# Kernel tuning notes

Measured on AMD Instinct MI355X. Metric: run time of the kernel, lower is better.

Reference implementation:

```python
import jax, jax.numpy as jnp
import numpy as np

D_MODEL = 256
N_HEAD = 8
D_FF = 1024
B = 8
N_PER = 4096
NQ = B * N_PER
L = 16
NEG_INF = -1e9
EPS = 1e-5


def layer_norm(x, g, b):
    mu = jnp.mean(x, axis=-1, keepdims=True)
    var = jnp.mean(jnp.square(x - mu), axis=-1, keepdims=True)
    return (x - mu) * jax.lax.rsqrt(var + EPS) * g + b


def setup_inputs() -> dict:
    key = jax.random.key(0)
    ks = jax.random.split(key, 20)
    s = 1.0 / np.sqrt(D_MODEL)
    sf = 1.0 / np.sqrt(D_FF)
    inp = {
        "src": jax.random.normal(ks[0], (NQ, D_MODEL), jnp.float32),
        "pos": jax.random.normal(ks[1], (NQ, D_MODEL), jnp.float32),
        # per-batch-relative neighbor indices in [-1, N_PER); -1 == invalid/padded
        "index_pair": jax.random.randint(ks[2], (NQ, L), 0, N_PER + 1, jnp.int32) - 1,
        "query_batch_cnt": jnp.full((B,), N_PER, jnp.int32),
        "key_batch_cnt": jnp.full((B,), N_PER, jnp.int32),
        "index_pair_batch": (jnp.arange(NQ, dtype=jnp.int32) // N_PER).astype(jnp.int32),
        "Wq": jax.random.normal(ks[3], (D_MODEL, D_MODEL), jnp.float32) * s,
        "bq": jnp.zeros((D_MODEL,), jnp.float32),
        "Wk": jax.random.normal(ks[4], (D_MODEL, D_MODEL), jnp.float32) * s,
        "bk": jnp.zeros((D_MODEL,), jnp.float32),
        "Wv": jax.random.normal(ks[5], (D_MODEL, D_MODEL), jnp.float32) * s,
        "bv": jnp.zeros((D_MODEL,), jnp.float32),
        "Wo": jax.random.normal(ks[6], (D_MODEL, D_MODEL), jnp.float32) * s,
        "bo": jnp.zeros((D_MODEL,), jnp.float32),
        "W1": jax.random.normal(ks[7], (D_MODEL, D_FF), jnp.float32) * s,
        "b1": jnp.zeros((D_FF,), jnp.float32),
        "W2": jax.random.normal(ks[8], (D_FF, D_MODEL), jnp.float32) * sf,
        "b2": jnp.zeros((D_MODEL,), jnp.float32),
        "g1": jnp.ones((D_MODEL,), jnp.float32),
        "be1": jnp.zeros((D_MODEL,), jnp.float32),
        "g2": jnp.ones((D_MODEL,), jnp.float32),
        "be2": jnp.zeros((D_MODEL,), jnp.float32),
    }
    return inp


def local_attn(q, k, v, index_pair, key_batch_cnt, index_pair_batch,
               Wq, bq, Wk, bk, Wv, bv, Wo, bo):
    H, hd = N_HEAD, D_MODEL // N_HEAD
    scale = 1.0 / np.sqrt(hd)
    qh = (q @ Wq + bq).reshape(NQ, H, hd) * scale        # [Nq,H,hd]
    kh = (k @ Wk + bk).reshape(NQ, H, hd)                # [Nk,H,hd] (Nk==Nq)
    vh = (v @ Wv + bv).reshape(NQ, H, hd)
    # start offset of each batch's keys in the stacked key tensor
    offs = jnp.cumsum(key_batch_cnt) - key_batch_cnt      # [B]
    valid = index_pair >= 0                               # [Nq,L]
    gidx = jnp.where(valid, index_pair + offs[index_pair_batch][:, None], 0)
    k_g = kh[gidx]                                        # [Nq,L,H,hd]
    v_g = vh[gidx]                                        # [Nq,L,H,hd]
    logits = jnp.einsum('nhd,nlhd->nhl', qh, k_g)         # [Nq,H,L]
    logits = jnp.where(valid[:, None, :], logits, NEG_INF)
    attn = jax.nn.softmax(logits, axis=-1)
    out = jnp.einsum('nhl,nlhd->nhd', attn, v_g).reshape(NQ, D_MODEL)
    return out @ Wo + bo


def reference(src, pos, index_pair, query_batch_cnt, key_batch_cnt, index_pair_batch,
              Wq, bq, Wk, bk, Wv, bv, Wo, bo, W1, b1, W2, b2, g1, be1, g2, be2):
    # forward_post (normalize_before=False), dropout==0 (eval)
    qk = src + pos
    src2 = local_attn(qk, qk, src, index_pair, key_batch_cnt, index_pair_batch,
                      Wq, bq, Wk, bk, Wv, bv, Wo, bo)
    x = layer_norm(src + src2, g1, be1)
    ff = jax.nn.relu(x @ W1 + b1) @ W2 + b2
    return layer_norm(x + ff, g2, be2)
```

## Files before the change

kernel.cpp:

```cpp
#include <hip/hip_runtime.h>
#include <hip/hip_bf16.h>
#include <cstdint>
#include <cstddef>

#define NQ_ 32768
#define DM_ 256
#define DFF_ 1024
#define LNB_ 16
#define NB_ 8

typedef __attribute__((ext_vector_type(4))) float f32x4;
typedef __attribute__((ext_vector_type(8))) short s16x8;

__device__ __forceinline__ float bf2f(ushort u) {
    union { unsigned int i; float f; } c; c.i = ((unsigned int)u) << 16; return c.f;
}
__device__ __forceinline__ ushort f2bf(float f) {
    union { float f; unsigned int i; } c; c.f = f;
    unsigned int x = c.i;
    return (ushort)((x + 0x7fffu + ((x >> 16) & 1u)) >> 16);
}


__global__ __launch_bounds__(256) void prep_qk(const float* __restrict__ src, const float* __restrict__ pos,
                                               ushort* __restrict__ qkb, ushort* __restrict__ srcb) {
    int i = (blockIdx.x * 256 + threadIdx.x) * 4;
    float4 s = *(const float4*)(src + i);
    float4 p = *(const float4*)(pos + i);
    ushort4 a, b;
    a.x = f2bf(s.x + p.x); a.y = f2bf(s.y + p.y); a.z = f2bf(s.z + p.z); a.w = f2bf(s.w + p.w);
    b.x = f2bf(s.x);       b.y = f2bf(s.y);       b.z = f2bf(s.z);       b.w = f2bf(s.w);
    *(ushort4*)(qkb + i) = a;
    *(ushort4*)(srcb + i) = b;
}

__global__ __launch_bounds__(256) void prep_weights(const float* __restrict__ Wq, const float* __restrict__ Wk,
                                                    const float* __restrict__ Wv, const float* __restrict__ Wo,
                                                    const float* __restrict__ W1, const float* __restrict__ W2,
                                                    const int* __restrict__ kbc,
                                                    const float* __restrict__ bq, const float* __restrict__ bk,
                                                    ushort* __restrict__ WqT, ushort* __restrict__ WkT,
                                                    ushort* __restrict__ WvT, ushort* __restrict__ WoT,
                                                    ushort* __restrict__ W1T, ushort* __restrict__ W2T,
                                                    int* __restrict__ offs, float* __restrict__ bias2) {
    const int b = blockIdx.x;
    const int t = threadIdx.x;
    if (b == 3072) {
        if (t == 0) { int a = 0; for (int i = 0; i < NB_; ++i) { offs[i] = a; a += kbc[i]; } }
        bias2[t] = bq[t];
        bias2[256 + t] = bk[t];
        return;
    }
    const float* W; ushort* Wt; int base, ks, ns;
    if (b < 1024) {
        const int sec = b >> 8;
        W  = sec == 0 ? Wq  : sec == 1 ? Wk  : sec == 2 ? Wv  : Wo;
        Wt = sec == 0 ? WqT : sec == 1 ? WkT : sec == 2 ? WvT : WoT;
        base = (b & 255) * 256; ks = 8; ns = 8;
    } else if (b < 2048) {
        W = W1; Wt = W1T; base = (b - 1024) * 256; ks = 8; ns = 10;
    } else {
        W = W2; Wt = W2T; base = (b - 2048) * 256; ks = 10; ns = 8;
    }
    const int i = base + t;
    const int n = i >> ks, k = i & ((1 << ks) - 1);
    Wt[i] = f2bf(W[(k << ns) + n]);
}


__device__ __forceinline__ void gld_lds16(const ushort* g, ushort* l) {
    __builtin_amdgcn_global_load_lds((const __attribute__((address_space(1))) void*)g,
                                     (__attribute__((address_space(3))) void*)l, 16, 0, 0);
}

template <bool RELU>
__global__ __launch_bounds__(256) void gemm_kernel(const ushort* __restrict__ A, const ushort* __restrict__ Bt,
                                                   const float* __restrict__ bias, ushort* __restrict__ C,
                                                   int M, int N, int K, float alpha) {
    __shared__ __align__(16) ushort As[2 * 128 * 32];
    __shared__ __align__(16) ushort Bs[2 * 128 * 32];
    const int tid = threadIdx.x;
    const int lane = tid & 63;
    const int wave = tid >> 6;
    const int wr = wave >> 1, wc = wave & 1;

    const int b = (int)(blockIdx.y * gridDim.x + blockIdx.x);
    const int idx = b >> 3;
    const int xt = (b & 7) * 32 + (idx & 31);
    const int yt = idx >> 5;
    const long m0 = (long)xt * 128;
    const long n0 = (long)yt * 128;

    f32x4 acc[4][4] = {};

    const int c0 = tid, c1 = tid + 256;
    const int ar0 = c0 >> 2, ac0 = c0 & 3;
    const int ar1 = c1 >> 2, ac1 = c1 & 3;
    const int as0 = (ac0 ^ ((ar0 >> 1) & 3)) * 8;
    const int as1 = (ac1 ^ ((ar1 >> 1) & 3)) * 8;
    const int la = lane & 15;
    const int sx = ((lane >> 4) ^ ((la >> 1) & 3)) * 8;

    const ushort* Ar0 = A + (m0 + ar0) * K + as0;
    const ushort* Ar1 = A + (m0 + ar1) * K + as1;
    const ushort* Br0 = Bt + (n0 + ar0) * K + as0;
    const ushort* Br1 = Bt + (n0 + ar1) * K + as1;

    const int nt = K >> 5;
    int boff = 0;
    gld_lds16(Ar0, As + c0 * 8);
    gld_lds16(Ar1, As + c1 * 8);
    gld_lds16(Br0, Bs + c0 * 8);
    gld_lds16(Br1, Bs + c1 * 8);

    for (int t = 0; t < nt; ++t) {
        if (t + 1 < nt) {
            const int kt = (t + 1) << 5;
            const int nb = boff ^ 4096;
            gld_lds16(Ar0 + kt, As + nb + c0 * 8);
            gld_lds16(Ar1 + kt, As + nb + c1 * 8);
            gld_lds16(Br0 + kt, Bs + nb + c0 * 8);
            gld_lds16(Br1 + kt, Bs + nb + c1 * 8);
            asm volatile("s_waitcnt vmcnt(4)" ::: "memory");
        } else {
            asm volatile("s_waitcnt vmcnt(0)" ::: "memory");
        }
        __builtin_amdgcn_s_barrier();
        s16x8 af[4], bfr[4];
#pragma unroll
        for (int m = 0; m < 4; ++m)
            af[m] = *(const s16x8*)(As + boff + (wr * 64 + m * 16 + la) * 32 + sx);
#pragma unroll
        for (int n = 0; n < 4; ++n)
            bfr[n] = *(const s16x8*)(Bs + boff + (wc * 64 + n * 16 + la) * 32 + sx);
        asm volatile("s_waitcnt lgkmcnt(0)" ::: "memory");
        __builtin_amdgcn_s_barrier();
#pragma unroll
        for (int m = 0; m < 4; ++m)
#pragma unroll
            for (int n = 0; n < 4; ++n)
                acc[m][n] = __builtin_amdgcn_mfma_f32_16x16x32_bf16(af[m], bfr[n], acc[m][n], 0, 0, 0);
        boff ^= 4096;
    }

#pragma unroll
    for (int n = 0; n < 4; ++n) {
        const long col = n0 + wc * 64 + n * 16 + la;
        const float bv = bias[col];
#pragma unroll
        for (int m = 0; m < 4; ++m) {
#pragma unroll
            for (int j = 0; j < 4; ++j) {
                const long row = m0 + wr * 64 + m * 16 + (lane >> 4) * 4 + j;
                float r = (acc[m][n][j] + bv) * alpha;
                if (RELU) r = fmaxf(r, 0.f);
                C[row * N + col] = f2bf(r);
            }
        }
    }
}


__global__ __launch_bounds__(256, 4) void attn_kernel(const ushort* __restrict__ QKb,
                                                      const ushort* __restrict__ Vb, const int* __restrict__ ipair,
                                                      const int* __restrict__ ipb, const int* __restrict__ offs,
                                                      ushort* __restrict__ Ob) {
    const int blk = (blockIdx.x & 7) * (NQ_ / 8 / 8) + (blockIdx.x >> 3);
    const int lane = threadIdx.x & 63;
    const int n = blk * 8 + (threadIdx.x >> 6) * 2 + (lane >> 5);
    const size_t hoff = (size_t)(lane & 31) * 8;

    float q[8];
    {
        s16x8 v = *(const s16x8*)(QKb + (size_t)n * 512 + hoff);
#pragma unroll
        for (int e = 0; e < 8; ++e) q[e] = bf2f((ushort)v[e]);
    }
    const int off = offs[ipb[n]];
    int gi[LNB_];
    float lg[LNB_];
#pragma unroll
    for (int j = 0; j < LNB_; ++j) {
        const int ip = ipair[n * LNB_ + j];
        const int g = ip >= 0 ? ip + off : 0;
        gi[j] = g;
        s16x8 v = *(const s16x8*)(QKb + (size_t)g * 512 + 256 + hoff);
        float p = 0.f;
#pragma unroll
        for (int e = 0; e < 8; ++e)
            p = fmaf(q[e], bf2f((ushort)v[e]), p);
        p += __shfl_xor(p, 1);
        p += __shfl_xor(p, 2);
        lg[j] = ip >= 0 ? p * 0.17677669529663688f : -1e9f;
    }
    float mx = lg[0];
#pragma unroll
    for (int j = 1; j < LNB_; ++j) mx = fmaxf(mx, lg[j]);
    float sum = 0.f, pw[LNB_];
#pragma unroll
    for (int j = 0; j < LNB_; ++j) { pw[j] = __expf(lg[j] - mx); sum += pw[j]; }
    const float inv = 1.f / sum;

    float acc[8] = {};
#pragma unroll
    for (int j = 0; j < LNB_; ++j) {
        s16x8 v = *(const s16x8*)(Vb + (size_t)gi[j] * DM_ + hoff);
        const float w = pw[j] * inv;
#pragma unroll
        for (int e = 0; e < 8; ++e)
            acc[e] = fmaf(w, bf2f((ushort)v[e]), acc[e]);
    }
    s16x8 o;
#pragma unroll
    for (int e = 0; e < 8; ++e) o[e] = (short)f2bf(acc[e]);
    *(s16x8*)(Ob + (size_t)n * DM_ + hoff) = o;
}


__global__ __launch_bounds__(256) void ln1_kernel(const ushort* __restrict__ a, const ushort* __restrict__ y,
                                                  const float* __restrict__ g, const float* __restrict__ be,
                                                  ushort* __restrict__ out) {
    const int row = blockIdx.x * 4 + (threadIdx.x >> 6);
    const int lane = threadIdx.x & 63;
    const int e = lane * 4;
    const size_t base = (size_t)row * DM_ + e;
    ushort4 av = *(const ushort4*)(a + base);
    ushort4 yv = *(const ushort4*)(y + base);
    float v0 = bf2f(av.x) + bf2f(yv.x), v1 = bf2f(av.y) + bf2f(yv.y);
    float v2 = bf2f(av.z) + bf2f(yv.z), v3 = bf2f(av.w) + bf2f(yv.w);
    float s = v0 + v1 + v2 + v3;
#pragma unroll
    for (int mk = 1; mk < 64; mk <<= 1) s += __shfl_xor(s, mk);
    const float mu = s * (1.f / 256.f);
    v0 -= mu; v1 -= mu; v2 -= mu; v3 -= mu;
    float qv = v0 * v0 + v1 * v1 + v2 * v2 + v3 * v3;
#pragma unroll
    for (int mk = 1; mk < 64; mk <<= 1) qv += __shfl_xor(qv, mk);
    const float r = rsqrtf(qv * (1.f / 256.f) + 1e-5f);
    ushort4 o;
    o.x = f2bf(v0 * r * g[e] + be[e]);
    o.y = f2bf(v1 * r * g[e + 1] + be[e + 1]);
    o.z = f2bf(v2 * r * g[e + 2] + be[e + 2]);
    o.w = f2bf(v3 * r * g[e + 3] + be[e + 3]);
    *(ushort4*)(out + base) = o;
}

__global__ __launch_bounds__(256) void ln2_kernel(const ushort* __restrict__ x, const ushort* __restrict__ f,
                                                  const float* __restrict__ g, const float* __restrict__ be,
                                                  float* __restrict__ out) {
    const int row = blockIdx.x * 4 + (threadIdx.x >> 6);
    const int lane = threadIdx.x & 63;
    const int e = lane * 4;
    const size_t base = (size_t)row * DM_ + e;
    ushort4 xv = *(const ushort4*)(x + base);
    ushort4 fv = *(const ushort4*)(f + base);
    float v0 = bf2f(xv.x) + bf2f(fv.x), v1 = bf2f(xv.y) + bf2f(fv.y);
    float v2 = bf2f(xv.z) + bf2f(fv.z), v3 = bf2f(xv.w) + bf2f(fv.w);
    float s = v0 + v1 + v2 + v3;
#pragma unroll
    for (int mk = 1; mk < 64; mk <<= 1) s += __shfl_xor(s, mk);
    const float mu = s * (1.f / 256.f);
    v0 -= mu; v1 -= mu; v2 -= mu; v3 -= mu;
    float qv = v0 * v0 + v1 * v1 + v2 * v2 + v3 * v3;
#pragma unroll
    for (int mk = 1; mk < 64; mk <<= 1) qv += __shfl_xor(qv, mk);
    const float r = rsqrtf(qv * (1.f / 256.f) + 1e-5f);
    float4 o;
    o.x = v0 * r * g[e] + be[e];
    o.y = v1 * r * g[e + 1] + be[e + 1];
    o.z = v2 * r * g[e + 2] + be[e + 2];
    o.w = v3 * r * g[e + 3] + be[e + 3];
    *(float4*)(out + base) = o;
}


extern "C" void kernel_launch(void* const* d_in, const int* in_sizes, int n_in,
                              void* d_out, int out_size, void* d_ws, size_t ws_size,
                              hipStream_t stream) {
    const float* src = (const float*)d_in[0];
    const float* pos = (const float*)d_in[1];
    const int* ipair = (const int*)d_in[2];
    const int* kbc   = (const int*)d_in[4];
    const int* ipb   = (const int*)d_in[5];
    const float* Wq = (const float*)d_in[6];  const float* bq = (const float*)d_in[7];
    const float* Wk = (const float*)d_in[8];  const float* bk = (const float*)d_in[9];
    const float* Wv = (const float*)d_in[10]; const float* bv = (const float*)d_in[11];
    const float* Wo = (const float*)d_in[12]; const float* bo = (const float*)d_in[13];
    const float* W1 = (const float*)d_in[14]; const float* b1 = (const float*)d_in[15];
    const float* W2 = (const float*)d_in[16]; const float* b2 = (const float*)d_in[17];
    const float* g1 = (const float*)d_in[18]; const float* be1 = (const float*)d_in[19];
    const float* g2 = (const float*)d_in[20]; const float* be2 = (const float*)d_in[21];

    char* ws = (char*)d_ws;
    const size_t SB = (size_t)NQ_ * DM_ * 2;
    ushort* qkb  = (ushort*)(ws);
    ushort* srcb = (ushort*)(ws + SB);
    ushort* QKb  = (ushort*)(ws + 2 * SB);
    ushort* Vb   = (ushort*)(ws + 4 * SB);
    ushort* fb   = (ushort*)(ws + 5 * SB);
    ushort* hb   = (ushort*)(ws);
    ushort* attno = qkb;
    ushort* yb    = (ushort*)(ws + 2 * SB);
    ushort* xb    = Vb;
    char* wb = ws + 6 * SB;
    ushort* WqT = (ushort*)(wb);
    ushort* WkT = (ushort*)(wb + 131072);
    ushort* WvT = (ushort*)(wb + 262144);
    ushort* WoT = (ushort*)(wb + 393216);
    ushort* W1T = (ushort*)(wb + 524288);
    ushort* W2T = (ushort*)(wb + 1048576);
    int* offs   = (int*)(wb + 1572864);
    float* bias2 = (float*)(wb + 1572864 + 64);

    prep_weights<<<3073, 256, 0, stream>>>(Wq, Wk, Wv, Wo, W1, W2, kbc, bq, bk,
                                           WqT, WkT, WvT, WoT, W1T, W2T, offs, bias2);
    prep_qk<<<NQ_ * DM_ / 4 / 256, 256, 0, stream>>>(src, pos, qkb, srcb);

    dim3 gqk(NQ_ / 128, 512 / 128);
    dim3 g256(NQ_ / 128, DM_ / 128);
    dim3 gff1(NQ_ / 128, DFF_ / 128);
    gemm_kernel<false><<<gqk, 256, 0, stream>>>(qkb, WqT, bias2, QKb, NQ_, 512, DM_, 1.f);
    gemm_kernel<false><<<g256, 256, 0, stream>>>(srcb, WvT, bv, Vb, NQ_, DM_, DM_, 1.f);
    attn_kernel<<<NQ_ / 8, 256, 0, stream>>>(QKb, Vb, ipair, ipb, offs, attno);
    gemm_kernel<false><<<g256, 256, 0, stream>>>(attno, WoT, bo, yb, NQ_, DM_, DM_, 1.f);
    ln1_kernel<<<NQ_ / 4, 256, 0, stream>>>(srcb, yb, g1, be1, xb);
    gemm_kernel<true><<<gff1, 256, 0, stream>>>(xb, W1T, b1, hb, NQ_, DFF_, DM_, 1.f);
    gemm_kernel<false><<<g256, 256, 0, stream>>>(hb, W2T, b2, fb, NQ_, DM_, DFF_, 1.f);
    ln2_kernel<<<NQ_ / 4, 256, 0, stream>>>(xb, fb, g2, be2, (float*)d_out);
}
```

Baseline: 184.6 us.

## Restructure GEMM so each wave owns an independent 64x64 tile without block barriers

The GEMM kernel drops the shared 128x128 block tile with double-buffered LDS and workgroup barriers. Each of the four waves now computes its own 64x64 output tile from a private LDS slice, with no s_barrier and a 1D swizzled grid. This removes block-level synchronisation and raises occupancy (launch bounds set to 3). In exchange it loses the software prefetch of the next K slice, since each iteration waits on vmcnt(0), and each A/B element is loaded by fewer consumers, which lowers reuse and increases global and L2 traffic.

```diff
diff --git a/kernel.cpp b/kernel.cpp
--- a/kernel.cpp
+++ b/kernel.cpp
@@ -74,84 +74,71 @@
 }
 
 template <bool RELU>
-__global__ __launch_bounds__(256) void gemm_kernel(const ushort* __restrict__ A, const ushort* __restrict__ Bt,
-                                                   const float* __restrict__ bias, ushort* __restrict__ C,
-                                                   int M, int N, int K, float alpha) {
-    __shared__ __align__(16) ushort As[2 * 128 * 32];
-    __shared__ __align__(16) ushort Bs[2 * 128 * 32];
+__global__ __launch_bounds__(256, 3) void gemm_kernel(const ushort* __restrict__ A, const ushort* __restrict__ Bt,
+                                                      const float* __restrict__ bias, ushort* __restrict__ C,
+                                                      int M, int N, int K, float alpha) {
+    __shared__ __align__(16) ushort lds[4 * 4096];
     const int tid = threadIdx.x;
     const int lane = tid & 63;
     const int wave = tid >> 6;
-    const int wr = wave >> 1, wc = wave & 1;
-
-    const int b = (int)(blockIdx.y * gridDim.x + blockIdx.x);
-    const int idx = b >> 3;
-    const int xt = (b & 7) * 32 + (idx & 31);
-    const int yt = idx >> 5;
-    const long m0 = (long)xt * 128;
-    const long n0 = (long)yt * 128;
-
-    f32x4 acc[4][4] = {};
-
-    const int c0 = tid, c1 = tid + 256;
-    const int ar0 = c0 >> 2, ac0 = c0 & 3;
-    const int ar1 = c1 >> 2, ac1 = c1 & 3;
-    const int as0 = (ac0 ^ ((ar0 >> 1) & 3)) * 8;
-    const int as1 = (ac1 ^ ((ar1 >> 1) & 3)) * 8;
+    ushort* ws_ = lds + wave * 4096;
+
+    const int G = (int)gridDim.x;
+    const int sb = ((int)blockIdx.x & 7) * (G >> 3) + ((int)blockIdx.x >> 3);
+    const int tile = sb * 4 + wave;
+    const int nt = N >> 6;
+    const int nsh = __ffs(nt) - 1;
+    const int mt = tile >> nsh;
+    const int ntl = tile & (nt - 1);
+    const long m0 = (long)mt * 64;
+    const long n0 = (long)ntl * 64;
+
+    const int l = lane;
+    const int srcc8 = ((l & 3) ^ ((l >> 3) & 3)) * 8;
+    const int rsub = l >> 2;
     const int la = lane & 15;
     const int sx = ((lane >> 4) ^ ((la >> 1) & 3)) * 8;
 
-    const ushort* Ar0 = A + (m0 + ar0) * K + as0;
-    const ushort* Ar1 = A + (m0 + ar1) * K + as1;
-    const ushort* Br0 = Bt + (n0 + ar0) * K + as0;
-    const ushort* Br1 = Bt + (n0 + ar1) * K + as1;
-
-    const int nt = K >> 5;
-    int boff = 0;
-    gld_lds16(Ar0, As + c0 * 8);
-    gld_lds16(Ar1, As + c1 * 8);
-    gld_lds16(Br0, Bs + c0 * 8);
-    gld_lds16(Br1, Bs + c1 * 8);
-
-    for (int t = 0; t < nt; ++t) {
-        if (t + 1 < nt) {
-            const int kt = (t + 1) << 5;
-            const int nb = boff ^ 4096;
-            gld_lds16(Ar0 + kt, As + nb + c0 * 8);
-            gld_lds16(Ar1 + kt, As + nb + c1 * 8);
-            gld_lds16(Br0 + kt, Bs + nb + c0 * 8);
-            gld_lds16(Br1 + kt, Bs + nb + c1 * 8);
-            asm volatile("s_waitcnt vmcnt(4)" ::: "memory");
-        } else {
-            asm volatile("s_waitcnt vmcnt(0)" ::: "memory");
-        }
-        __builtin_amdgcn_s_barrier();
+    const ushort* A0 = A + m0 * K + srcc8;
+    const ushort* B0 = Bt + n0 * K + srcc8;
+
+    f32x4 acc[4][4] = {};
+
+    for (int kt = 0; kt < K; kt += 32) {
+#pragma unroll
+        for (int j = 0; j < 4; ++j)
+            gld_lds16(A0 + (j * 16 + rsub) * K + kt, ws_ + j * 512 + l * 8);
+#pragma unroll
+        for (int j = 0; j < 4; ++j)
+            gld_lds16(B0 + (j * 16 + rsub) * K + kt, ws_ + 2048 + j * 512 + l * 8);
+        asm volatile("s_waitcnt vmcnt(0)" ::: "memory");
+        __builtin_amdgcn_sched_barrier(0);
         s16x8 af[4], bfr[4];
 #pragma unroll
         for (int m = 0; m < 4; ++m)
-            af[m] = *(const s16x8*)(As + boff + (wr * 64 + m * 16 + la) * 32 + sx);
+            af[m] = *(const s16x8*)(ws_ + (m * 16 + la) * 32 + sx);
 #pragma unroll
         for (int n = 0; n < 4; ++n)
-            bfr[n] = *(const s16x8*)(Bs + boff + (wc * 64 + n * 16 + la) * 32 + sx);
+            bfr[n] = *(const s16x8*)(ws_ + 2048 + (n * 16 + la) * 32 + sx);
         asm volatile("s_waitcnt lgkmcnt(0)" ::: "memory");
-        __builtin_amdgcn_s_barrier();
+        __builtin_amdgcn_sched_barrier(0);
 #pragma unroll
         for (int m = 0; m < 4; ++m)
 #pragma unroll
             for (int n = 0; n < 4; ++n)
                 acc[m][n] = __builtin_amdgcn_mfma_f32_16x16x32_bf16(af[m], bfr[n], acc[m][n], 0, 0, 0);
-        boff ^= 4096;
-    }
-
+    }
+
+    const int rg = (lane >> 4) * 4;
 #pragma unroll
     for (int n = 0; n < 4; ++n) {
-        const long col = n0 + wc * 64 + n * 16 + la;
+        const long col = n0 + n * 16 + la;
         const float bv = bias[col];
 #pragma unroll
         for (int m = 0; m < 4; ++m) {
 #pragma unroll
             for (int j = 0; j < 4; ++j) {
-                const long row = m0 + wr * 64 + m * 16 + (lane >> 4) * 4 + j;
+                const long row = m0 + m * 16 + rg + j;
                 float r = (acc[m][n][j] + bv) * alpha;
                 if (RELU) r = fmaxf(r, 0.f);
                 C[row * N + col] = f2bf(r);
@@ -316,15 +303,15 @@
                                            WqT, WkT, WvT, WoT, W1T, W2T, offs, bias2);
     prep_qk<<<NQ_ * DM_ / 4 / 256, 256, 0, stream>>>(src, pos, qkb, srcb);
 
-    dim3 gqk(NQ_ / 128, 512 / 128);
-    dim3 g256(NQ_ / 128, DM_ / 128);
-    dim3 gff1(NQ_ / 128, DFF_ / 128);
-    gemm_kernel<false><<<gqk, 256, 0, stream>>>(qkb, WqT, bias2, QKb, NQ_, 512, DM_, 1.f);
+    const int gQK  = (NQ_ / 64) * (512 / 64) / 4;
+    const int g256 = (NQ_ / 64) * (DM_ / 64) / 4;
+    const int gFF1 = (NQ_ / 64) * (DFF_ / 64) / 4;
+    gemm_kernel<false><<<gQK, 256, 0, stream>>>(qkb, WqT, bias2, QKb, NQ_, 512, DM_, 1.f);
     gemm_kernel<false><<<g256, 256, 0, stream>>>(srcb, WvT, bv, Vb, NQ_, DM_, DM_, 1.f);
     attn_kernel<<<NQ_ / 8, 256, 0, stream>>>(QKb, Vb, ipair, ipb, offs, attno);
     gemm_kernel<false><<<g256, 256, 0, stream>>>(attno, WoT, bo, yb, NQ_, DM_, DM_, 1.f);
     ln1_kernel<<<NQ_ / 4, 256, 0, stream>>>(srcb, yb, g1, be1, xb);
-    gemm_kernel<true><<<gff1, 256, 0, stream>>>(xb, W1T, b1, hb, NQ_, DFF_, DM_, 1.f);
+    gemm_kernel<true><<<gFF1, 256, 0, stream>>>(xb, W1T, b1, hb, NQ_, DFF_, DM_, 1.f);
     gemm_kernel<false><<<g256, 256, 0, stream>>>(hb, W2T, b2, fb, NQ_, DM_, DFF_, 1.f);
     ln2_kernel<<<NQ_ / 4, 256, 0, stream>>>(xb, fb, g2, be2, (float*)d_out);
 }
```

After: 189.3 us. 2.6% more time.

## Fuse residual add and LayerNorm into the output-projection and FFN2 GEMM epilogues

Applied to the files above, without the earlier changes.

Adds a GEMM kernel whose block tile covers 64 full rows of the 256-wide output, so the residual add and LayerNorm run in the epilogue through a shared-memory cross-wave reduction. It replaces the Wo GEMM plus ln1 and the W2 GEMM plus ln2, removing two launches and the bf16 round trips of the intermediate outputs. The trade-offs are a narrower M tile with no double buffering, non-vectorized scalar residual loads and output stores, and variance computed as E[x^2]-mu^2, which is less numerically stable.

```diff
diff --git a/kernel.cpp b/kernel.cpp
--- a/kernel.cpp
+++ b/kernel.cpp
@@ -161,6 +161,107 @@
 }
 
 
+template <bool F32OUT>
+__global__ __launch_bounds__(256) void gemm_ln_kernel(const ushort* __restrict__ A, const ushort* __restrict__ Bt,
+                                                      const float* __restrict__ bias,
+                                                      const ushort* __restrict__ resid,
+                                                      const float* __restrict__ g, const float* __restrict__ be,
+                                                      void* __restrict__ outv, int K) {
+    __shared__ __align__(16) ushort As[64 * 32];
+    __shared__ __align__(16) ushort Bs[256 * 32];
+    __shared__ float red_s[4][64];
+    __shared__ float red_q[4][64];
+    const int tid = threadIdx.x;
+    const int lane = tid & 63;
+    const int wave = tid >> 6;
+    const long m0 = (long)blockIdx.x * 64;
+
+    const int ca = tid;
+    const ushort* Arow = A + (m0 + (ca >> 2)) * K + ((ca & 3) ^ ((ca >> 3) & 3)) * 8;
+    const ushort* Brow[4];
+#pragma unroll
+    for (int i = 0; i < 4; ++i) {
+        const int cb = tid + 256 * i;
+        Brow[i] = Bt + (long)(cb >> 2) * K + ((cb & 3) ^ ((cb >> 3) & 3)) * 8;
+    }
+    const int la = lane & 15;
+    const int sx = ((lane >> 4) ^ ((la >> 1) & 3)) * 8;
+
+    f32x4 acc[4][4] = {};
+
+    for (int kt = 0; kt < K; kt += 32) {
+        gld_lds16(Arow + kt, As + ca * 8);
+#pragma unroll
+        for (int i = 0; i < 4; ++i)
+            gld_lds16(Brow[i] + kt, Bs + (tid + 256 * i) * 8);
+        __syncthreads();
+        s16x8 af[4], bfr[4];
+#pragma unroll
+        for (int m = 0; m < 4; ++m)
+            af[m] = *(const s16x8*)(As + (m * 16 + la) * 32 + sx);
+#pragma unroll
+        for (int n = 0; n < 4; ++n)
+            bfr[n] = *(const s16x8*)(Bs + (wave * 64 + n * 16 + la) * 32 + sx);
+#pragma unroll
+        for (int m = 0; m < 4; ++m)
+#pragma unroll
+            for (int n = 0; n < 4; ++n)
+                acc[m][n] = __builtin_amdgcn_mfma_f32_16x16x32_bf16(af[m], bfr[n], acc[m][n], 0, 0, 0);
+        __syncthreads();
+    }
+
+    const int rg4 = (lane >> 4) * 4;
+    float bv[4];
+#pragma unroll
+    for (int n = 0; n < 4; ++n) bv[n] = bias[wave * 64 + n * 16 + la];
+
+#pragma unroll
+    for (int m = 0; m < 4; ++m) {
+#pragma unroll
+        for (int j = 0; j < 4; ++j) {
+            const int lr = m * 16 + rg4 + j;
+            float s = 0.f, q = 0.f;
+#pragma unroll
+            for (int n = 0; n < 4; ++n) {
+                const int col = wave * 64 + n * 16 + la;
+                float v = acc[m][n][j] + bv[n] + bf2f(resid[(m0 + lr) * DM_ + col]);
+                acc[m][n][j] = v;
+                s += v; q += v * v;
+            }
+#pragma unroll
+            for (int mk = 1; mk < 16; mk <<= 1) { s += __shfl_xor(s, mk); q += __shfl_xor(q, mk); }
+            if (la == 0) { red_s[wave][lr] = s; red_q[wave][lr] = q; }
+        }
+    }
+    __syncthreads();
+
+    float gv[4], bev[4];
+#pragma unroll
+    for (int n = 0; n < 4; ++n) {
+        const int col = wave * 64 + n * 16 + la;
+        gv[n] = g[col]; bev[n] = be[col];
+    }
+#pragma unroll
+    for (int m = 0; m < 4; ++m) {
+#pragma unroll
+        for (int j = 0; j < 4; ++j) {
+            const int lr = m * 16 + rg4 + j;
+            const float s = red_s[0][lr] + red_s[1][lr] + red_s[2][lr] + red_s[3][lr];
+            const float q = red_q[0][lr] + red_q[1][lr] + red_q[2][lr] + red_q[3][lr];
+            const float mu = s * (1.f / 256.f);
+            const float rsig = rsqrtf(q * (1.f / 256.f) - mu * mu + 1e-5f);
+#pragma unroll
+            for (int n = 0; n < 4; ++n) {
+                const int col = wave * 64 + n * 16 + la;
+                const float r = (acc[m][n][j] - mu) * rsig * gv[n] + bev[n];
+                if (F32OUT) ((float*)outv)[(m0 + lr) * DM_ + col] = r;
+                else        ((ushort*)outv)[(m0 + lr) * DM_ + col] = f2bf(r);
+            }
+        }
+    }
+}
+
+
 __global__ __launch_bounds__(256, 4) void attn_kernel(const ushort* __restrict__ QKb,
                                                       const ushort* __restrict__ Vb, const int* __restrict__ ipair,
                                                       const int* __restrict__ ipb, const int* __restrict__ offs,
@@ -214,63 +315,6 @@
 #pragma unroll
     for (int e = 0; e < 8; ++e) o[e] = (short)f2bf(acc[e]);
     *(s16x8*)(Ob + (size_t)n * DM_ + hoff) = o;
-}
-
-
-__global__ __launch_bounds__(256) void ln1_kernel(const ushort* __restrict__ a, const ushort* __restrict__ y,
-                                                  const float* __restrict__ g, const float* __restrict__ be,
-                                                  ushort* __restrict__ out) {
-    const int row = blockIdx.x * 4 + (threadIdx.x >> 6);
-    const int lane = threadIdx.x & 63;
-    const int e = lane * 4;
-    const size_t base = (size_t)row * DM_ + e;
-    ushort4 av = *(const ushort4*)(a + base);
-    ushort4 yv = *(const ushort4*)(y + base);
-    float v0 = bf2f(av.x) + bf2f(yv.x), v1 = bf2f(av.y) + bf2f(yv.y);
-    float v2 = bf2f(av.z) + bf2f(yv.z), v3 = bf2f(av.w) + bf2f(yv.w);
-    float s = v0 + v1 + v2 + v3;
-#pragma unroll
-    for (int mk = 1; mk < 64; mk <<= 1) s += __shfl_xor(s, mk);
-    const float mu = s * (1.f / 256.f);
-    v0 -= mu; v1 -= mu; v2 -= mu; v3 -= mu;
-    float qv = v0 * v0 + v1 * v1 + v2 * v2 + v3 * v3;
-#pragma unroll
-    for (int mk = 1; mk < 64; mk <<= 1) qv += __shfl_xor(qv, mk);
-    const float r = rsqrtf(qv * (1.f / 256.f) + 1e-5f);
-    ushort4 o;
-    o.x = f2bf(v0 * r * g[e] + be[e]);
-    o.y = f2bf(v1 * r * g[e + 1] + be[e + 1]);
-    o.z = f2bf(v2 * r * g[e + 2] + be[e + 2]);
-    o.w = f2bf(v3 * r * g[e + 3] + be[e + 3]);
-    *(ushort4*)(out + base) = o;
-}
-
-__global__ __launch_bounds__(256) void ln2_kernel(const ushort* __restrict__ x, const ushort* __restrict__ f,
-                                                  const float* __restrict__ g, const float* __restrict__ be,
-                                                  float* __restrict__ out) {
-    const int row = blockIdx.x * 4 + (threadIdx.x >> 6);
-    const int lane = threadIdx.x & 63;
-    const int e = lane * 4;
-    const size_t base = (size_t)row * DM_ + e;
-    ushort4 xv = *(const ushort4*)(x + base);
-    ushort4 fv = *(const ushort4*)(f + base);
-    float v0 = bf2f(xv.x) + bf2f(fv.x), v1 = bf2f(xv.y) + bf2f(fv.y);
-    float v2 = bf2f(xv.z) + bf2f(fv.z), v3 = bf2f(xv.w) + bf2f(fv.w);
-    float s = v0 + v1 + v2 + v3;
-#pragma unroll
-    for (int mk = 1; mk < 64; mk <<= 1) s += __shfl_xor(s, mk);
-    const float mu = s * (1.f / 256.f);
-    v0 -= mu; v1 -= mu; v2 -= mu; v3 -= mu;
-    float qv = v0 * v0 + v1 * v1 + v2 * v2 + v3 * v3;
-#pragma unroll
-    for (int mk = 1; mk < 64; mk <<= 1) qv += __shfl_xor(qv, mk);
-    const float r = rsqrtf(qv * (1.f / 256.f) + 1e-5f);
-    float4 o;
-    o.x = v0 * r * g[e] + be[e];
-    o.y = v1 * r * g[e + 1] + be[e + 1];
-    o.z = v2 * r * g[e + 2] + be[e + 2];
-    o.w = v3 * r * g[e + 3] + be[e + 3];
-    *(float4*)(out + base) = o;
 }
 
 
@@ -297,10 +341,8 @@
     ushort* srcb = (ushort*)(ws + SB);
     ushort* QKb  = (ushort*)(ws + 2 * SB);
     ushort* Vb   = (ushort*)(ws + 4 * SB);
-    ushort* fb   = (ushort*)(ws + 5 * SB);
     ushort* hb   = (ushort*)(ws);
     ushort* attno = qkb;
-    ushort* yb    = (ushort*)(ws + 2 * SB);
     ushort* xb    = Vb;
     char* wb = ws + 6 * SB;
     ushort* WqT = (ushort*)(wb);
@@ -322,9 +364,7 @@
     gemm_kernel<false><<<gqk, 256, 0, stream>>>(qkb, WqT, bias2, QKb, NQ_, 512, DM_, 1.f);
     gemm_kernel<false><<<g256, 256, 0, stream>>>(srcb, WvT, bv, Vb, NQ_, DM_, DM_, 1.f);
     attn_kernel<<<NQ_ / 8, 256, 0, stream>>>(QKb, Vb, ipair, ipb, offs, attno);
-    gemm_kernel<false><<<g256, 256, 0, stream>>>(attno, WoT, bo, yb, NQ_, DM_, DM_, 1.f);
-    ln1_kernel<<<NQ_ / 4, 256, 0, stream>>>(srcb, yb, g1, be1, xb);
+    gemm_ln_kernel<false><<<NQ_ / 64, 256, 0, stream>>>(attno, WoT, bo, srcb, g1, be1, (void*)xb, DM_);
     gemm_kernel<true><<<gff1, 256, 0, stream>>>(xb, W1T, b1, hb, NQ_, DFF_, DM_, 1.f);
-    gemm_kernel<false><<<g256, 256, 0, stream>>>(hb, W2T, b2, fb, NQ_, DM_, DFF_, 1.f);
-    ln2_kernel<<<NQ_ / 4, 256, 0, stream>>>(xb, fb, g2, be2, (float*)d_out);
-}
+    gemm_ln_kernel<true><<<NQ_ / 64, 256, 0, stream>>>(hb, W2T, b2, xb, g2, be2, d_out, DFF_);
+}
```

Measured after the change: 182.3 us. Within noise of the previous version (-1.2%).
